# Optimization experiments

Hardware: AMD Instinct MI355X
Metric: run time of the kernel (lower is better)

The kernel has to match this reference:

```python
import jax, jax.numpy as jnp
import numpy as np

T = 4.0          # kd_T
PATCH_NUM = 16
MASK_NUM = 4
P = PATCH_NUM - MASK_NUM  # 12
B = 4096
D_IN = 640
D = 128


def embed(x, w1, b1, w2, b2):
    # Linear -> ReLU -> Linear -> L2 normalize over features
    h = jax.nn.relu(x @ w1.T + b1)
    y = h @ w2.T + b2
    norm = jnp.sqrt(jnp.sum(y * y, axis=1, keepdims=True))
    return y / norm


def kl_rows(y_s, y_t):
    # Matches KLDiv: kl_div(log_softmax(y_s/T), softmax(y_t/T), 'batchmean') * T^2
    # over dim=0 of a 1-D vector -> sum / D. Vectorized over leading dims.
    ls = jax.nn.log_softmax(y_s / T, axis=-1)
    lt = jax.nn.log_softmax(y_t / T, axis=-1)
    pt = jnp.exp(lt)
    return jnp.sum(pt * (lt - ls), axis=-1) / y_s.shape[-1] * (T * T)


def setup_inputs() -> dict:
    key = jax.random.key(0)
    ks = jax.random.split(key, 11)
    return {
        "ebg": jax.random.normal(ks[0], (B, D_IN), jnp.float32),
        "ebp": jax.random.normal(ks[1], (P * B, D_IN), jnp.float32),
        "labelsg": jax.random.randint(ks[2], (B,), 0, 64),
        "glo_w1": jax.random.normal(ks[3], (D, D_IN), jnp.float32) * 0.04,
        "glo_b1": jax.random.normal(ks[4], (D,), jnp.float32) * 0.02,
        "glo_w2": jax.random.normal(ks[5], (D, D), jnp.float32) * 0.09,
        "glo_b2": jax.random.normal(ks[6], (D,), jnp.float32) * 0.02,
        "pat_w1": jax.random.normal(ks[7], (D, D_IN), jnp.float32) * 0.04,
        "pat_b1": jax.random.normal(ks[8], (D,), jnp.float32) * 0.02,
        "pat_w2": jax.random.normal(ks[9], (D, D), jnp.float32) * 0.09,
        "pat_b2": jax.random.normal(ks[10], (D,), jnp.float32) * 0.02,
    }


def reference(ebg, ebp, labelsg, glo_w1, glo_b1, glo_w2, glo_b2,
              pat_w1, pat_b1, pat_w2, pat_b2):
    sg = jax.lax.stop_gradient
    g = embed(ebg, glo_w1, glo_b1, glo_w2, glo_b2)          # [B, D]
    p = embed(ebp, pat_w1, pat_b1, pat_w2, pat_b2)          # [P*B, D]
    p = p.reshape(P, B, D)
    p_bar = p.mean(axis=0)                                  # [B, D]

    # soft_dil_loss: symmetric KL between g[b] and p_bar[b]
    dil = jnp.sum(kl_rows(g, sg(p_bar)) + kl_rows(p_bar, sg(g)))

    # soft_dcl_loss: symmetric KL between (g[b]-p[b,l])^2 and (p_bar[b]-p[b,l])^2
    p_bt = jnp.transpose(p, (1, 0, 2))                      # [B, P, D]
    d1 = (g[:, None, :] - p_bt) ** 2                        # [B, P, D]
    d2 = (p_bar[:, None, :] - p_bt) ** 2                    # [B, P, D]
    dcl = jnp.sum(kl_rows(d1, sg(d2)) + kl_rows(d2, sg(d1))) / P

    return (dil, dcl)
```

## Files before the change

### kernel.cpp

```cpp
#include <hip/hip_runtime.h>
#include <math.h>

#define B_    4096
#define DIN   640
#define DD    128
#define PP    12
#define INV_T 0.25f

typedef __bf16 bft;
typedef __attribute__((ext_vector_type(8))) __bf16 bf16x8;
typedef __attribute__((ext_vector_type(4))) float fx4;

__device__ __forceinline__ void gload16(const float* gp, float* lp) {
  __builtin_amdgcn_global_load_lds(
      (const __attribute__((address_space(1))) unsigned int*)gp,
      (__attribute__((address_space(3))) unsigned int*)lp,
      16, 0, 0);
}

__global__ __launch_bounds__(256) void prep_kernel(
    const float* __restrict__ gw1, const float* __restrict__ pw1,
    const float* __restrict__ gw2, const float* __restrict__ pw2,
    bft* __restrict__ w1hg, bft* __restrict__ w1lg,
    bft* __restrict__ w1hp, bft* __restrict__ w1lp,
    bft* __restrict__ w2hg, bft* __restrict__ w2lg,
    bft* __restrict__ w2hp, bft* __restrict__ w2lp)
{
  int idx = blockIdx.x * 256 + threadIdx.x;
  const float* src; bft *dh, *dl; int off;
  if (idx < 81920)       { src = gw1; dh = w1hg; dl = w1lg; off = idx; }
  else if (idx < 163840) { src = pw1; dh = w1hp; dl = w1lp; off = idx - 81920; }
  else if (idx < 180224) { src = gw2; dh = w2hg; dl = w2lg; off = idx - 163840; }
  else                   { src = pw2; dh = w2hp; dl = w2lp; off = idx - 180224; }
  float x = src[off];
  bft h = (bft)x;
  dh[off] = h;
  dl[off] = (bft)(x - (float)h);
}

__global__ __launch_bounds__(256, 2) void embed_kernel(
    const float* __restrict__ ebg, const float* __restrict__ ebp,
    const bft* __restrict__ w1hg, const bft* __restrict__ w1lg, const float* __restrict__ b1g,
    const bft* __restrict__ w2hg, const bft* __restrict__ w2lg, const float* __restrict__ b2g,
    const bft* __restrict__ w1hp, const bft* __restrict__ w1lp, const float* __restrict__ b1p,
    const bft* __restrict__ w2hp, const bft* __restrict__ w2lp, const float* __restrict__ b2p,
    float* __restrict__ outg, float* __restrict__ outp)
{
  __shared__ bft hsm[2 * 128 * 128];
  float* xbase = (float*)hsm;
  bft* hhi = hsm;
  bft* hlo = hsm + 128 * 128;
  float* halfsq = (float*)hsm;

  const int t = threadIdx.x;
  const int w = t >> 6, lane = t & 63;
  const int wm = w >> 1, wn = w & 1;
  const int ln = lane & 15, quad = lane >> 4;

  const float *X, *B1, *B2;
  const bft *W1H, *W1L, *W2H, *W2L;
  float* Y;
  long m0;
  if (blockIdx.x < 32) {
    X = ebg; W1H = w1hg; W1L = w1lg; B1 = b1g; W2H = w2hg; W2L = w2lg; B2 = b2g;
    Y = outg; m0 = (long)blockIdx.x * 128;
  } else {
    X = ebp; W1H = w1hp; W1L = w1lp; B1 = b1p; W2H = w2hp; W2L = w2lp; B2 = b2p;
    Y = outp; m0 = (long)(blockIdx.x - 32) * 128;
  }

  const int srow = lane >> 3;
  const int skq  = (lane & 7) ^ srow;
  const float* xsrc = X + (size_t)(m0 + w * 32 + srow) * DIN + skq * 4;
  const int ldst = w * 32 * 32 + lane * 4;

#define GLX(bufp, k0)                                        \
  _Pragma("unroll")                                          \
  for (int j = 0; j < 4; j++)                                \
    gload16(xsrc + (size_t)j * 8 * DIN + (k0), (bufp) + ldst + j * 8 * 32);

  const int s0 = ((quad << 1) ^ (ln & 7));

  const bft *p1h[4], *p1l[4];
#pragma unroll
  for (int nt = 0; nt < 4; nt++) {
    int n = wn * 64 + nt * 16 + ln;
    p1h[nt] = W1H + (size_t)n * DIN + quad * 8;
    p1l[nt] = W1L + (size_t)n * DIN + quad * 8;
  }

  fx4 acc[4][4];
#pragma unroll
  for (int mt = 0; mt < 4; mt++)
#pragma unroll
    for (int nt = 0; nt < 4; nt++) acc[mt][nt] = (fx4){0.f, 0.f, 0.f, 0.f};

#define LOADW(wh, wl, koff)                                \
  _Pragma("unroll")                                        \
  for (int nt = 0; nt < 4; nt++) {                         \
    wh[nt] = *(const bf16x8*)(p1h[nt] + (koff));           \
    wl[nt] = *(const bf16x8*)(p1l[nt] + (koff));           \
  }

#define PH1CHUNK(bufp, wh, wl)                                                         \
  {                                                                                    \
    bf16x8 ah[4], al[4];                                                               \
    _Pragma("unroll")                                                                  \
    for (int mt = 0; mt < 4; mt++) {                                                   \
      const float* rp = (bufp) + (wm * 64 + mt * 16 + ln) * 32;                        \
      fx4 x0 = *(const fx4*)(rp + s0 * 4);                                             \
      fx4 x1 = *(const fx4*)(rp + (s0 ^ 1) * 4);                                       \
      _Pragma("unroll")                                                                \
      for (int j = 0; j < 4; j++) {                                                    \
        float xv = x0[j];                                                              \
        bft hh = (bft)xv;                                                              \
        ah[mt][j] = hh;                                                                \
        al[mt][j] = (bft)(xv - (float)hh);                                             \
        float yv = x1[j];                                                              \
        bft hh2 = (bft)yv;                                                             \
        ah[mt][4 + j] = hh2;                                                           \
        al[mt][4 + j] = (bft)(yv - (float)hh2);                                        \
      }                                                                                \
    }                                                                                  \
    _Pragma("unroll")                                                                  \
    for (int mt = 0; mt < 4; mt++)                                                     \
      _Pragma("unroll")                                                                \
      for (int nt = 0; nt < 4; nt++) {                                                 \
        acc[mt][nt] = __builtin_amdgcn_mfma_f32_16x16x32_bf16(ah[mt], wh[nt], acc[mt][nt], 0, 0, 0); \
        acc[mt][nt] = __builtin_amdgcn_mfma_f32_16x16x32_bf16(al[mt], wh[nt], acc[mt][nt], 0, 0, 0); \
        acc[mt][nt] = __builtin_amdgcn_mfma_f32_16x16x32_bf16(ah[mt], wl[nt], acc[mt][nt], 0, 0, 0); \
      }                                                                                \
  }

  bf16x8 wha[4], wla[4], whb[4], wlb[4];
  GLX(xbase, 0)
  GLX(xbase + 4096, 32)
  GLX(xbase + 8192, 64)
  LOADW(wha, wla, 0)

#define HALFSTEP(c, WCH, WCL, WNH, WNL, VMTOK)                              \
  {                                                                          \
    const int kn_ = ((c) + 1 < 20) ? ((c) + 1) * 32 : 0;                     \
    LOADW(WNH, WNL, kn_)                                                     \
    asm volatile("s_waitcnt vmcnt(" VMTOK ") lgkmcnt(0)" ::: "memory");      \
    __builtin_amdgcn_s_barrier();                                            \
    __builtin_amdgcn_sched_barrier(0);                                       \
    const int kp_ = ((c) + 3 < 20) ? ((c) + 3) * 32 : 0;                     \
    float* pslot_ = xbase + ((((c) + 3) & 3) << 12);                         \
    GLX(pslot_, kp_)                                                         \
    PH1CHUNK(xbase + ((((c) & 3)) << 12), WCH, WCL)                          \
  }

  HALFSTEP(0, wha, wla, whb, wlb, "24")
  for (int kc = 1; kc < 19; kc += 2) {
    HALFSTEP(kc,     whb, wlb, wha, wla, "32")
    HALFSTEP(kc + 1, wha, wla, whb, wlb, "32")
  }
  HALFSTEP(19, whb, wlb, wha, wla, "32")

  __syncthreads();

#pragma unroll
  for (int nt = 0; nt < 4; nt++) {
    float bv = B1[wn * 64 + nt * 16 + ln];
    int c8 = wn * 8 + nt * 2 + (ln >> 3);
    int c7 = ln & 7;
#pragma unroll
    for (int mt = 0; mt < 4; mt++) {
#pragma unroll
      for (int r = 0; r < 4; r++) {
        float v = fmaxf(acc[mt][nt][r] + bv, 0.f);
        bft h = (bft)v;
        bft l = (bft)(v - (float)h);
        int m = wm * 64 + mt * 16 + quad * 4 + r;
        int addr = m * 128 + ((c8 ^ (m & 15)) << 3) + c7;
        hhi[addr] = h;
        hlo[addr] = l;
      }
    }
  }

  const bft *p2h[4], *p2l[4];
#pragma unroll
  for (int nt = 0; nt < 4; nt++) {
    int n = wn * 64 + nt * 16 + ln;
    p2h[nt] = W2H + (size_t)n * DD + quad * 8;
    p2l[nt] = W2L + (size_t)n * DD + quad * 8;
  }
  fx4 acc2[4][4];
#pragma unroll
  for (int nt = 0; nt < 4; nt++) {
    float bv = B2[wn * 64 + nt * 16 + ln];
#pragma unroll
    for (int mt = 0; mt < 4; mt++) acc2[mt][nt] = (fx4){bv, bv, bv, bv};
  }

#define LOADW2(wh, wl, koff)                               \
  _Pragma("unroll")                                        \
  for (int nt = 0; nt < 4; nt++) {                         \
    wh[nt] = *(const bf16x8*)(p2h[nt] + (koff));           \
    wl[nt] = *(const bf16x8*)(p2l[nt] + (koff));           \
  }

#define PH2CHUNK(kcv, wh, wl)                                                          \
  {                                                                                    \
    bf16x8 ah2[4], al2[4];                                                             \
    _Pragma("unroll")                                                                  \
    for (int mt = 0; mt < 4; mt++) {                                                   \
      int m = wm * 64 + mt * 16 + ln;                                                  \
      int c8 = ((kcv) * 4 + quad) ^ (m & 15);                                          \
      ah2[mt] = *(const bf16x8*)&hhi[m * 128 + (c8 << 3)];                             \
      al2[mt] = *(const bf16x8*)&hlo[m * 128 + (c8 << 3)];                             \
    }                                                                                  \
    _Pragma("unroll")                                                                  \
    for (int mt = 0; mt < 4; mt++)                                                     \
      _Pragma("unroll")                                                                \
      for (int nt = 0; nt < 4; nt++) {                                                 \
        acc2[mt][nt] = __builtin_amdgcn_mfma_f32_16x16x32_bf16(ah2[mt], wh[nt], acc2[mt][nt], 0, 0, 0); \
        acc2[mt][nt] = __builtin_amdgcn_mfma_f32_16x16x32_bf16(al2[mt], wh[nt], acc2[mt][nt], 0, 0, 0); \
        acc2[mt][nt] = __builtin_amdgcn_mfma_f32_16x16x32_bf16(ah2[mt], wl[nt], acc2[mt][nt], 0, 0, 0); \
      }                                                                                \
  }

  bf16x8 q2ha[4], q2la[4], q2hb[4], q2lb[4];
  LOADW2(q2ha, q2la, 0)
  __syncthreads();
  LOADW2(q2hb, q2lb, 32)
  PH2CHUNK(0, q2ha, q2la)
  LOADW2(q2ha, q2la, 64)
  PH2CHUNK(1, q2hb, q2lb)
  LOADW2(q2hb, q2lb, 96)
  PH2CHUNK(2, q2ha, q2la)
  PH2CHUNK(3, q2hb, q2lb)
  __syncthreads();

#pragma unroll
  for (int mt = 0; mt < 4; mt++) {
#pragma unroll
    for (int r = 0; r < 4; r++) {
      float s = 0.f;
#pragma unroll
      for (int nt = 0; nt < 4; nt++) { float v = acc2[mt][nt][r]; s += v * v; }
      s += __shfl_xor(s, 1, 64);
      s += __shfl_xor(s, 2, 64);
      s += __shfl_xor(s, 4, 64);
      s += __shfl_xor(s, 8, 64);
      if (ln == 0) halfsq[(wm * 64 + mt * 16 + quad * 4 + r) * 2 + wn] = s;
    }
  }
  __syncthreads();
#pragma unroll
  for (int mt = 0; mt < 4; mt++) {
#pragma unroll
    for (int r = 0; r < 4; r++) {
      int row = wm * 64 + mt * 16 + quad * 4 + r;
      float rinv = 1.0f / sqrtf(halfsq[row * 2] + halfsq[row * 2 + 1]);
#pragma unroll
      for (int nt = 0; nt < 4; nt++)
        Y[(m0 + row) * DD + wn * 64 + nt * 16 + ln] = acc2[mt][nt][r] * rinv;
    }
  }
}

__device__ __forceinline__ float sym_kl_row(float au0, float au1, float av0, float av1)
{
  float eu0 = __expf(au0), eu1 = __expf(au1);
  float ev0 = __expf(av0), ev1 = __expf(av1);
  float su = eu0 + eu1, sv = ev0 + ev1;
#pragma unroll
  for (int o = 32; o > 0; o >>= 1) {
    su += __shfl_xor(su, o, 64);
    sv += __shfl_xor(sv, o, 64);
  }
  float ru = 1.0f / su, rv = 1.0f / sv;
  float d0 = au0 - av0, d1 = au1 - av1;
  float part = (eu0 * ru - ev0 * rv) * d0 + (eu1 * ru - ev1 * rv) * d1;
#pragma unroll
  for (int o = 32; o > 0; o >>= 1) part += __shfl_xor(part, o, 64);
  return part;
}

__global__ __launch_bounds__(256) void loss_kernel(
    const float* __restrict__ g, const float* __restrict__ p,
    float* __restrict__ pdil, float* __restrict__ pdcl)
{
  __shared__ float wd[4], wc[4];
  int w = threadIdx.x >> 6, lane = threadIdx.x & 63;
  int b = blockIdx.x * 4 + w;
  float2 pl[PP];
  float sx = 0.f, sy = 0.f;
#pragma unroll
  for (int l = 0; l < PP; l++) {
    pl[l] = *(const float2*)&p[((size_t)l * B_ + b) * DD + lane * 2];
    sx += pl[l].x; sy += pl[l].y;
  }
  sx *= (1.0f / PP); sy *= (1.0f / PP);
  float2 gv = *(const float2*)&g[(size_t)b * DD + lane * 2];

  float dil = sym_kl_row(gv.x * INV_T, gv.y * INV_T, sx * INV_T, sy * INV_T) * 0.125f;

  float dcl = 0.f;
#pragma unroll
  for (int l = 0; l < PP; l++) {
    float u0 = (gv.x - pl[l].x) * (gv.x - pl[l].x) * INV_T;
    float u1 = (gv.y - pl[l].y) * (gv.y - pl[l].y) * INV_T;
    float v0 = (sx - pl[l].x) * (sx - pl[l].x) * INV_T;
    float v1 = (sy - pl[l].y) * (sy - pl[l].y) * INV_T;
    dcl += sym_kl_row(u0, u1, v0, v1);
  }
  dcl *= (1.0f / 96.0f);

  if (lane == 0) { wd[w] = dil; wc[w] = dcl; }
  __syncthreads();
  if (threadIdx.x == 0) pdil[blockIdx.x] = wd[0] + wd[1] + wd[2] + wd[3];
  if (threadIdx.x == 1) pdcl[blockIdx.x] = wc[0] + wc[1] + wc[2] + wc[3];
}

__global__ __launch_bounds__(256) void final_kernel(const float* __restrict__ pdil,
                                                    const float* __restrict__ pdcl,
                                                    float* __restrict__ out)
{
  __shared__ float red[8];
  int t = threadIdx.x;
  float s0 = 0.f, s1 = 0.f;
  for (int i = t; i < 1024; i += 256) { s0 += pdil[i]; s1 += pdcl[i]; }
#pragma unroll
  for (int o = 32; o > 0; o >>= 1) {
    s0 += __shfl_xor(s0, o, 64);
    s1 += __shfl_xor(s1, o, 64);
  }
  int wid = t >> 6, lane = t & 63;
  if (lane == 0) { red[wid] = s0; red[4 + wid] = s1; }
  __syncthreads();
  if (t == 0) out[0] = red[0] + red[1] + red[2] + red[3];
  if (t == 1) out[1] = red[4] + red[5] + red[6] + red[7];
}

extern "C" void kernel_launch(void* const* d_in, const int* in_sizes, int n_in,
                              void* d_out, int out_size, void* d_ws, size_t ws_size,
                              hipStream_t stream)
{
  const float* ebg = (const float*)d_in[0];
  const float* ebp = (const float*)d_in[1];
  const float* gw1 = (const float*)d_in[3];
  const float* gb1 = (const float*)d_in[4];
  const float* gw2 = (const float*)d_in[5];
  const float* gb2 = (const float*)d_in[6];
  const float* pw1 = (const float*)d_in[7];
  const float* pb1 = (const float*)d_in[8];
  const float* pw2 = (const float*)d_in[9];
  const float* pb2 = (const float*)d_in[10];
  float* out = (float*)d_out;

  float* ws   = (float*)d_ws;
  float* g    = ws;
  float* p    = g + (size_t)B_ * DD;
  float* pdil = p + (size_t)PP * B_ * DD;
  float* pdcl = pdil + 1024;
  bft* wb     = (bft*)(pdcl + 1024);
  bft* w1hg = wb;                 bft* w1lg = w1hg + 81920;
  bft* w1hp = w1lg + 81920;       bft* w1lp = w1hp + 81920;
  bft* w2hg = w1lp + 81920;       bft* w2lg = w2hg + 16384;
  bft* w2hp = w2lg + 16384;       bft* w2lp = w2hp + 16384;

  prep_kernel<<<768, 256, 0, stream>>>(gw1, pw1, gw2, pw2,
                                       w1hg, w1lg, w1hp, w1lp,
                                       w2hg, w2lg, w2hp, w2lp);
  embed_kernel<<<416, 256, 0, stream>>>(ebg, ebp,
                                        w1hg, w1lg, gb1, w2hg, w2lg, gb2,
                                        w1hp, w1lp, pb1, w2hp, w2lp, pb2,
                                        g, p);
  loss_kernel<<<B_ / 4, 256, 0, stream>>>(g, p, pdil, pdcl);
  final_kernel<<<1, 256, 0, stream>>>(pdil, pdcl, out);
}
```

Before: 265.1 us.

## Pre-swizzle weights into MFMA fragment layout and store patches batch-major

The prep kernel now writes the hi/lo bf16 weight splits into a fragment-ordered layout, so each lane's 16-byte load of a weight fragment is contiguous and coalesced instead of strided by row. The embed kernel stores patch embeddings as [B, P, D] rather than [P, B, D], so the loss kernel reads the 12 patches of one batch row from a contiguous region. The trade-off is more index arithmetic in prep, with each thread doing 8 strided reads, and scattered output row writes in embed.

```diff
diff --git a/kernel.cpp b/kernel.cpp
--- a/kernel.cpp
+++ b/kernel.cpp
@@ -21,32 +21,57 @@
 __global__ __launch_bounds__(256) void prep_kernel(
     const float* __restrict__ gw1, const float* __restrict__ pw1,
     const float* __restrict__ gw2, const float* __restrict__ pw2,
-    bft* __restrict__ w1hg, bft* __restrict__ w1lg,
-    bft* __restrict__ w1hp, bft* __restrict__ w1lp,
-    bft* __restrict__ w2hg, bft* __restrict__ w2lg,
-    bft* __restrict__ w2hp, bft* __restrict__ w2lp)
-{
-  int idx = blockIdx.x * 256 + threadIdx.x;
-  const float* src; bft *dh, *dl; int off;
-  if (idx < 81920)       { src = gw1; dh = w1hg; dl = w1lg; off = idx; }
-  else if (idx < 163840) { src = pw1; dh = w1hp; dl = w1lp; off = idx - 81920; }
-  else if (idx < 180224) { src = gw2; dh = w2hg; dl = w2lg; off = idx - 163840; }
-  else                   { src = pw2; dh = w2hp; dl = w2lp; off = idx - 180224; }
-  float x = src[off];
-  bft h = (bft)x;
-  dh[off] = h;
-  dl[off] = (bft)(x - (float)h);
+    bft* __restrict__ w1fg, bft* __restrict__ w1fp,
+    bft* __restrict__ w2fg, bft* __restrict__ w2fp)
+{
+  int id = blockIdx.x * 256 + threadIdx.x;
+  const float* src;
+  bft* dst;
+  int nt, kc, hl, lane, kstride;
+  if (id < 40960) {
+    const bool isg = (id < 20480);
+    int f = isg ? id : (id - 20480);
+    src = isg ? gw1 : pw1;
+    dst = isg ? w1fg : w1fp;
+    lane = f & 63;
+    int q2 = f >> 6;
+    hl = q2 & 1;
+    int q3 = q2 >> 1;
+    kc = q3 % 20; nt = q3 / 20;
+    kstride = DIN;
+    dst += ((size_t)(nt * 20 + kc) * 2 + hl) * 512 + lane * 8;
+  } else {
+    const bool isg = (id < 45056);
+    int f = isg ? (id - 40960) : (id - 45056);
+    src = isg ? gw2 : pw2;
+    dst = isg ? w2fg : w2fp;
+    lane = f & 63;
+    int q2 = f >> 6;
+    hl = q2 & 1;
+    int q3 = q2 >> 1;
+    kc = q3 & 3; nt = q3 >> 2;
+    kstride = DD;
+    dst += ((size_t)(nt * 4 + kc) * 2 + hl) * 512 + lane * 8;
+  }
+  int ln = lane & 15, quad = lane >> 4;
+  const float* s = src + (size_t)(nt * 16 + ln) * kstride + kc * 32 + quad * 8;
+#pragma unroll
+  for (int e = 0; e < 8; e++) {
+    float x = s[e];
+    bft h = (bft)x;
+    dst[e] = hl ? (bft)(x - (float)h) : h;
+  }
 }
 
 __global__ __launch_bounds__(256, 2) void embed_kernel(
     const float* __restrict__ ebg, const float* __restrict__ ebp,
-    const bft* __restrict__ w1hg, const bft* __restrict__ w1lg, const float* __restrict__ b1g,
-    const bft* __restrict__ w2hg, const bft* __restrict__ w2lg, const float* __restrict__ b2g,
-    const bft* __restrict__ w1hp, const bft* __restrict__ w1lp, const float* __restrict__ b1p,
-    const bft* __restrict__ w2hp, const bft* __restrict__ w2lp, const float* __restrict__ b2p,
+    const bft* __restrict__ w1fg, const float* __restrict__ b1g,
+    const bft* __restrict__ w2fg, const float* __restrict__ b2g,
+    const bft* __restrict__ w1fp, const float* __restrict__ b1p,
+    const bft* __restrict__ w2fp, const float* __restrict__ b2p,
     float* __restrict__ outg, float* __restrict__ outp)
 {
-  __shared__ bft hsm[2 * 128 * 128];
+  __shared__ __align__(16) bft hsm[2 * 128 * 128];
   float* xbase = (float*)hsm;
   bft* hhi = hsm;
   bft* hlo = hsm + 128 * 128;
@@ -58,14 +83,15 @@
   const int ln = lane & 15, quad = lane >> 4;
 
   const float *X, *B1, *B2;
-  const bft *W1H, *W1L, *W2H, *W2L;
+  const bft *W1F, *W2F;
   float* Y;
   long m0;
-  if (blockIdx.x < 32) {
-    X = ebg; W1H = w1hg; W1L = w1lg; B1 = b1g; W2H = w2hg; W2L = w2lg; B2 = b2g;
+  const bool isg = (blockIdx.x < 32);
+  if (isg) {
+    X = ebg; W1F = w1fg; B1 = b1g; W2F = w2fg; B2 = b2g;
     Y = outg; m0 = (long)blockIdx.x * 128;
   } else {
-    X = ebp; W1H = w1hp; W1L = w1lp; B1 = b1p; W2H = w2hp; W2L = w2lp; B2 = b2p;
+    X = ebp; W1F = w1fp; B1 = b1p; W2F = w2fp; B2 = b2p;
     Y = outp; m0 = (long)(blockIdx.x - 32) * 128;
   }
 
@@ -81,13 +107,10 @@
 
   const int s0 = ((quad << 1) ^ (ln & 7));
 
-  const bft *p1h[4], *p1l[4];
-#pragma unroll
-  for (int nt = 0; nt < 4; nt++) {
-    int n = wn * 64 + nt * 16 + ln;
-    p1h[nt] = W1H + (size_t)n * DIN + quad * 8;
-    p1l[nt] = W1L + (size_t)n * DIN + quad * 8;
-  }
+  const bft* p1f[4];
+#pragma unroll
+  for (int nt = 0; nt < 4; nt++)
+    p1f[nt] = W1F + (size_t)(wn * 4 + nt) * 20480 + lane * 8;
 
   fx4 acc[4][4];
 #pragma unroll
@@ -95,11 +118,11 @@
 #pragma unroll
     for (int nt = 0; nt < 4; nt++) acc[mt][nt] = (fx4){0.f, 0.f, 0.f, 0.f};
 
-#define LOADW(wh, wl, koff)                                \
+#define LOADW(wh, wl, kcv)                                 \
   _Pragma("unroll")                                        \
   for (int nt = 0; nt < 4; nt++) {                         \
-    wh[nt] = *(const bf16x8*)(p1h[nt] + (koff));           \
-    wl[nt] = *(const bf16x8*)(p1l[nt] + (koff));           \
+    wh[nt] = *(const bf16x8*)(p1f[nt] + (kcv) * 1024);     \
+    wl[nt] = *(const bf16x8*)(p1f[nt] + (kcv) * 1024 + 512); \
   }
 
 #define PH1CHUNK(bufp, wh, wl)                                                         \
@@ -140,7 +163,7 @@
 
 #define HALFSTEP(c, WCH, WCL, WNH, WNL, VMTOK)                              \
   {                                                                          \
-    const int kn_ = ((c) + 1 < 20) ? ((c) + 1) * 32 : 0;                     \
+    const int kn_ = ((c) + 1 < 20) ? ((c) + 1) : 0;                          \
     LOADW(WNH, WNL, kn_)                                                     \
     asm volatile("s_waitcnt vmcnt(" VMTOK ") lgkmcnt(0)" ::: "memory");      \
     __builtin_amdgcn_s_barrier();                                            \
@@ -180,13 +203,11 @@
     }
   }
 
-  const bft *p2h[4], *p2l[4];
-#pragma unroll
-  for (int nt = 0; nt < 4; nt++) {
-    int n = wn * 64 + nt * 16 + ln;
-    p2h[nt] = W2H + (size_t)n * DD + quad * 8;
-    p2l[nt] = W2L + (size_t)n * DD + quad * 8;
-  }
+  const bft* p2f[4];
+#pragma unroll
+  for (int nt = 0; nt < 4; nt++)
+    p2f[nt] = W2F + (size_t)(wn * 4 + nt) * 4096 + lane * 8;
+
   fx4 acc2[4][4];
 #pragma unroll
   for (int nt = 0; nt < 4; nt++) {
@@ -195,11 +216,11 @@
     for (int mt = 0; mt < 4; mt++) acc2[mt][nt] = (fx4){bv, bv, bv, bv};
   }
 
-#define LOADW2(wh, wl, koff)                               \
+#define LOADW2(wh, wl, kcv)                                \
   _Pragma("unroll")                                        \
   for (int nt = 0; nt < 4; nt++) {                         \
-    wh[nt] = *(const bf16x8*)(p2h[nt] + (koff));           \
-    wl[nt] = *(const bf16x8*)(p2l[nt] + (koff));           \
+    wh[nt] = *(const bf16x8*)(p2f[nt] + (kcv) * 1024);     \
+    wl[nt] = *(const bf16x8*)(p2f[nt] + (kcv) * 1024 + 512); \
   }
 
 #define PH2CHUNK(kcv, wh, wl)                                                          \
@@ -225,11 +246,11 @@
   bf16x8 q2ha[4], q2la[4], q2hb[4], q2lb[4];
   LOADW2(q2ha, q2la, 0)
   __syncthreads();
-  LOADW2(q2hb, q2lb, 32)
+  LOADW2(q2hb, q2lb, 1)
   PH2CHUNK(0, q2ha, q2la)
-  LOADW2(q2ha, q2la, 64)
+  LOADW2(q2ha, q2la, 2)
   PH2CHUNK(1, q2hb, q2lb)
-  LOADW2(q2hb, q2lb, 96)
+  LOADW2(q2hb, q2lb, 3)
   PH2CHUNK(2, q2ha, q2la)
   PH2CHUNK(3, q2hb, q2lb)
   __syncthreads();
@@ -255,9 +276,18 @@
     for (int r = 0; r < 4; r++) {
       int row = wm * 64 + mt * 16 + quad * 4 + r;
       float rinv = 1.0f / sqrtf(halfsq[row * 2] + halfsq[row * 2 + 1]);
-#pragma unroll
-      for (int nt = 0; nt < 4; nt++)
-        Y[(m0 + row) * DD + wn * 64 + nt * 16 + ln] = acc2[mt][nt][r] * rinv;
+      long R = m0 + row;
+#pragma unroll
+      for (int nt = 0; nt < 4; nt++) {
+        float val = acc2[mt][nt][r] * rinv;
+        int col = wn * 64 + nt * 16 + ln;
+        if (isg) {
+          Y[R * DD + col] = val;
+        } else {
+          long l_ = R >> 12, b_ = R & 4095;
+          Y[(b_ * PP + l_) * DD + col] = val;
+        }
+      }
     }
   }
 }
@@ -291,7 +321,7 @@
   float sx = 0.f, sy = 0.f;
 #pragma unroll
   for (int l = 0; l < PP; l++) {
-    pl[l] = *(const float2*)&p[((size_t)l * B_ + b) * DD + lane * 2];
+    pl[l] = *(const float2*)&p[((size_t)b * PP + l) * DD + lane * 2];
     sx += pl[l].x; sy += pl[l].y;
   }
   sx *= (1.0f / PP); sy *= (1.0f / PP);
@@ -357,18 +387,17 @@
   float* p    = g + (size_t)B_ * DD;
   float* pdil = p + (size_t)PP * B_ * DD;
   float* pdcl = pdil + 1024;
-  bft* wb     = (bft*)(pdcl + 1024);
-  bft* w1hg = wb;                 bft* w1lg = w1hg + 81920;
-  bft* w1hp = w1lg + 81920;       bft* w1lp = w1hp + 81920;
-  bft* w2hg = w1lp + 81920;       bft* w2lg = w2hg + 16384;
-  bft* w2hp = w2lg + 16384;       bft* w2lp = w2hp + 16384;
-
-  prep_kernel<<<768, 256, 0, stream>>>(gw1, pw1, gw2, pw2,
-                                       w1hg, w1lg, w1hp, w1lp,
-                                       w2hg, w2lg, w2hp, w2lp);
+  bft* wb   = (bft*)(pdcl + 1024);
+  bft* w1fg = wb;
+  bft* w1fp = w1fg + 163840;
+  bft* w2fg = w1fp + 163840;
+  bft* w2fp = w2fg + 32768;
+
+  prep_kernel<<<192, 256, 0, stream>>>(gw1, pw1, gw2, pw2,
+                                       w1fg, w1fp, w2fg, w2fp);
   embed_kernel<<<416, 256, 0, stream>>>(ebg, ebp,
-                                        w1hg, w1lg, gb1, w2hg, w2lg, gb2,
-                                        w1hp, w1lp, pb1, w2hp, w2lp, pb2,
+                                        w1fg, gb1, w2fg, gb2,
+                                        w1fp, pb1, w2fp, pb2,
                                         g, p);
   loss_kernel<<<B_ / 4, 256, 0, stream>>>(g, p, pdil, pdcl);
   final_kernel<<<1, 256, 0, stream>>>(pdil, pdcl, out);
```

After: 246.0 us. 1.08x faster.
